# Kernel tuning notes

Hardware: AMD Instinct MI355X
Metric: run time of the kernel (lower is better)

The kernel has to match this reference:

```python
import jax, jax.numpy as jnp
import numpy as np

EPS_BN = 1e-5
EPS_NORM = 1e-12
TOP_K = 512


def _conv(x, w):
    # NCHW conv, stride 1, SAME padding (ultralytics Conv autopad)
    return jax.lax.conv_general_dilated(x, w, (1, 1), 'SAME',
                                        dimension_numbers=('NCHW', 'OIHW', 'NCHW'))


def _bn(x, g, b, m, v):
    # inference-mode BatchNorm2d
    inv = jax.lax.rsqrt(v + EPS_BN)
    return (x - m[None, :, None, None]) * (g * inv)[None, :, None, None] + b[None, :, None, None]


def _descriptor(feat, p):
    (w_dr, g_dr, b_dr, m_dr, v_dr,
     w_d1, g_d1, b_d1, m_d1, v_d1,
     g_e, b_e, m_e, v_e,
     w_d2, g_d2, b_d2, m_d2, v_d2) = p
    # dim_reduce: Conv(channel, channel//2, 1) = conv+BN+SiLU
    x = jax.nn.silu(_bn(_conv(feat, w_dr), g_dr, b_dr, m_dr, v_dr))
    # descriptor: Conv(c/2, c/2, 3) + BN + ReLU + Conv(c/2, c/4, 1)
    x = jax.nn.silu(_bn(_conv(x, w_d1), g_d1, b_d1, m_d1, v_d1))
    x = jax.nn.relu(_bn(x, g_e, b_e, m_e, v_e))
    x = jax.nn.silu(_bn(_conv(x, w_d2), g_d2, b_d2, m_d2, v_d2))
    return x


def _keypoints(desc):
    b, c, h, w = desc.shape
    resp = jnp.sqrt(jnp.sum(desc * desc, axis=1)).reshape(b, h * w)  # L2 norm over channels
    _, idx = jax.lax.top_k(resp, TOP_K)                              # [b, K]
    y = (idx // w).astype(desc.dtype) / (h - 1) * 2 - 1
    x = (idx % w).astype(desc.dtype) / (w - 1) * 2 - 1
    return jnp.stack([x, y], axis=-1), idx                           # [b,K,2], [b,K]


def _forward(rgb_feat, ir_feat, params):
    rgb_desc = _descriptor(rgb_feat, params)
    ir_desc = _descriptor(ir_feat, params)

    kp1, idx1 = _keypoints(rgb_desc)
    kp2, idx2 = _keypoints(ir_desc)

    b, c, h, w = rgb_desc.shape
    hw = h * w
    d1 = rgb_desc.reshape(b, c, hw)
    d2 = ir_desc.reshape(b, c, hw)
    d1 = d1 / jnp.maximum(jnp.linalg.norm(d1, axis=1, keepdims=True), EPS_NORM)
    d2 = d2 / jnp.maximum(jnp.linalg.norm(d2, axis=1, keepdims=True), EPS_NORM)
    corr = jnp.einsum('bcn,bcm->bnm', d1, d2)     # [b, hw, hw]
    soft = jax.nn.softmax(corr, axis=-1)

    # scalar matching weight per keypoint pair (gather at keypoint locations)
    bidx = jnp.arange(b)[:, None]
    wts = soft[bidx, idx1, idx2]                  # [b, K]

    # vectorized DLT: A rows, two per point, weighted
    x1, y1 = kp1[..., 0], kp1[..., 1]
    x2, y2 = kp2[..., 0], kp2[..., 1]
    one = jnp.ones_like(x1)
    zer = jnp.zeros_like(x1)
    r1 = jnp.stack([x1, y1, one, zer, zer, zer, -x2 * x1, -x2 * y1, -x2], axis=-1)
    r2 = jnp.stack([zer, zer, zer, x1, y1, one, -y2 * x1, -y2 * y1, -y2], axis=-1)
    A = jnp.stack([r1, r2], axis=2) * wts[:, :, None, None]   # [b,K,2,9]
    A = A.reshape(b, 2 * TOP_K, 9)

    _, _, Vh = jnp.linalg.svd(A, full_matrices=False)          # Vh: [b,9,9]
    # torch.svd returns V; original takes V[-1] == last COLUMN of jax Vh
    H = Vh[:, :, -1].reshape(b, 3, 3)
    return H, rgb_desc, ir_desc


def setup_inputs() -> dict:
    key = jax.random.key(0)
    ks = jax.random.split(key, 8)
    B, C, Hh, Ww = 2, 256, 64, 64
    c2, c4 = C // 2, C // 4
    f32 = jnp.float32

    def bn_params(c):
        return (jnp.ones((c,), f32), jnp.zeros((c,), f32),
                jnp.zeros((c,), f32), jnp.ones((c,), f32))

    g_dr, b_dr, m_dr, v_dr = bn_params(c2)
    g_d1, b_d1, m_d1, v_d1 = bn_params(c2)
    g_e, b_e, m_e, v_e = bn_params(c2)
    g_d2, b_d2, m_d2, v_d2 = bn_params(c4)

    return {
        'rgb_feat': jax.random.normal(ks[0], (B, C, Hh, Ww), f32),
        'ir_feat': jax.random.normal(ks[1], (B, C, Hh, Ww), f32),
        'w_dr': jax.random.normal(ks[2], (c2, C, 1, 1), f32) * 0.05,
        'g_dr': g_dr, 'b_dr': b_dr, 'm_dr': m_dr, 'v_dr': v_dr,
        'w_d1': jax.random.normal(ks[3], (c2, c2, 3, 3), f32) * 0.05,
        'g_d1': g_d1, 'b_d1': b_d1, 'm_d1': m_d1, 'v_d1': v_d1,
        'g_e': g_e, 'b_e': b_e, 'm_e': m_e, 'v_e': v_e,
        'w_d2': jax.random.normal(ks[4], (c4, c2, 1, 1), f32) * 0.05,
        'g_d2': g_d2, 'b_d2': b_d2, 'm_d2': m_d2, 'v_d2': v_d2,
    }


def reference(rgb_feat, ir_feat,
              w_dr, g_dr, b_dr, m_dr, v_dr,
              w_d1, g_d1, b_d1, m_d1, v_d1,
              g_e, b_e, m_e, v_e,
              w_d2, g_d2, b_d2, m_d2, v_d2):
    params = (w_dr, g_dr, b_dr, m_dr, v_dr,
              w_d1, g_d1, b_d1, m_d1, v_d1,
              g_e, b_e, m_e, v_e,
              w_d2, g_d2, b_d2, m_d2, v_d2)
    return _forward(rgb_feat, ir_feat, params)
```

## Files before the change

kernel.cpp:

```cpp
#include <hip/hip_runtime.h>
#include <math.h>


#define HW4 4096
#define NIMG 4

#define OFF_X1   0L
#define OFF_X2   (OFF_X1 + 4L*128*4096)
#define OFF_RESP (OFF_X2 + 4L*128*4096)
#define OFF_INVN (OFF_RESP + 4L*4096)
#define OFF_TOPI (OFF_INVN + 4L*4096)
#define OFF_WTS  (OFF_TOPI + 4L*512)
#define OFF_A    (OFF_WTS + 2L*512)
#define OFF_QN   OFF_X1
#define OFF_PART (OFF_X1 + 65536L)

#define NSPLIT 16

__device__ __forceinline__ float silu_f(float y) { return y / (1.f + expf(-y)); }

__global__ __launch_bounds__(256) void fm_conv1(
    const float* __restrict__ rgb, const float* __restrict__ ir,
    const float* __restrict__ w, const float* __restrict__ g,
    const float* __restrict__ bb, const float* __restrict__ mm,
    const float* __restrict__ vv, float* __restrict__ x1) {
  __shared__ float wl[256*8];
  int bid = blockIdx.x;
  int pblk = bid & 3, ocg = (bid >> 2) & 15, img = bid >> 6;
  int oc0 = ocg * 8;
  int tid = threadIdx.x;
  const float* src = (img < 2) ? (rgb + (long)img*256*HW4) : (ir + (long)(img-2)*256*HW4);
  for (int i = tid; i < 2048; i += 256) {
    int o = i & 7, ic = i >> 3;
    wl[i] = w[(oc0 + o)*256 + ic];
  }
  __syncthreads();
  int p0 = pblk*1024 + tid*4;
  float acc[8][4];
  #pragma unroll
  for (int o = 0; o < 8; ++o)
    #pragma unroll
    for (int j = 0; j < 4; ++j) acc[o][j] = 0.f;
  #pragma unroll 4
  for (int ic = 0; ic < 256; ++ic) {
    float4 v = *(const float4*)(src + (long)ic*HW4 + p0);
    float4 wa = *(const float4*)&wl[ic*8];
    float4 wb = *(const float4*)&wl[ic*8 + 4];
    acc[0][0] = fmaf(wa.x, v.x, acc[0][0]); acc[0][1] = fmaf(wa.x, v.y, acc[0][1]);
    acc[0][2] = fmaf(wa.x, v.z, acc[0][2]); acc[0][3] = fmaf(wa.x, v.w, acc[0][3]);
    acc[1][0] = fmaf(wa.y, v.x, acc[1][0]); acc[1][1] = fmaf(wa.y, v.y, acc[1][1]);
    acc[1][2] = fmaf(wa.y, v.z, acc[1][2]); acc[1][3] = fmaf(wa.y, v.w, acc[1][3]);
    acc[2][0] = fmaf(wa.z, v.x, acc[2][0]); acc[2][1] = fmaf(wa.z, v.y, acc[2][1]);
    acc[2][2] = fmaf(wa.z, v.z, acc[2][2]); acc[2][3] = fmaf(wa.z, v.w, acc[2][3]);
    acc[3][0] = fmaf(wa.w, v.x, acc[3][0]); acc[3][1] = fmaf(wa.w, v.y, acc[3][1]);
    acc[3][2] = fmaf(wa.w, v.z, acc[3][2]); acc[3][3] = fmaf(wa.w, v.w, acc[3][3]);
    acc[4][0] = fmaf(wb.x, v.x, acc[4][0]); acc[4][1] = fmaf(wb.x, v.y, acc[4][1]);
    acc[4][2] = fmaf(wb.x, v.z, acc[4][2]); acc[4][3] = fmaf(wb.x, v.w, acc[4][3]);
    acc[5][0] = fmaf(wb.y, v.x, acc[5][0]); acc[5][1] = fmaf(wb.y, v.y, acc[5][1]);
    acc[5][2] = fmaf(wb.y, v.z, acc[5][2]); acc[5][3] = fmaf(wb.y, v.w, acc[5][3]);
    acc[6][0] = fmaf(wb.z, v.x, acc[6][0]); acc[6][1] = fmaf(wb.z, v.y, acc[6][1]);
    acc[6][2] = fmaf(wb.z, v.z, acc[6][2]); acc[6][3] = fmaf(wb.z, v.w, acc[6][3]);
    acc[7][0] = fmaf(wb.w, v.x, acc[7][0]); acc[7][1] = fmaf(wb.w, v.y, acc[7][1]);
    acc[7][2] = fmaf(wb.w, v.z, acc[7][2]); acc[7][3] = fmaf(wb.w, v.w, acc[7][3]);
  }
  #pragma unroll
  for (int o = 0; o < 8; ++o) {
    int oc = oc0 + o;
    float inv = 1.f / sqrtf(vv[oc] + 1e-5f);
    float sc = g[oc]*inv;
    float4 r;
    r.x = silu_f((acc[o][0] - mm[oc])*sc + bb[oc]);
    r.y = silu_f((acc[o][1] - mm[oc])*sc + bb[oc]);
    r.z = silu_f((acc[o][2] - mm[oc])*sc + bb[oc]);
    r.w = silu_f((acc[o][3] - mm[oc])*sc + bb[oc]);
    *(float4*)(x1 + ((long)img*128 + oc)*HW4 + p0) = r;
  }
}

#define C3_TW 72
#define C3_TR 18
__global__ __launch_bounds__(256) void fm_conv3(
    const float* __restrict__ x1, const float* __restrict__ w,
    const float* __restrict__ g1, const float* __restrict__ b1,
    const float* __restrict__ m1, const float* __restrict__ v1,
    const float* __restrict__ ge, const float* __restrict__ be,
    const float* __restrict__ me, const float* __restrict__ ve,
    float* __restrict__ x2) {
  __shared__ float t[2][4][C3_TR*C3_TW];
  __shared__ float wl[2][4][9][8];
  int bid = blockIdx.x;
  int rt = bid & 3, ocg = (bid >> 2) & 15, img = bid >> 6;
  int oc0 = ocg * 8;
  int y0 = rt * 16;
  int tid = threadIdx.x;
  int ly = tid >> 4;
  int lx = tid & 15;
  int x0 = lx * 4;
  const float* xim = x1 + (long)img*128*HW4;

  for (int i = tid; i < 1152; i += 256) {
    int buf = i / 576, rem = i - buf*576;
    int q = rem / 144, rem2 = rem - q*144;
    int rr = rem2 >> 3, e = rem2 & 7;
    t[buf][q][rr*C3_TW + ((e < 4) ? e : 64 + e)] = 0.f;
  }

  int lofs4[5];
  int goff4[5];
  #pragma unroll
  for (int t5 = 0; t5 < 5; ++t5) {
    int i = tid + 256*t5;
    if (i < 1152) {
      int q = i / 288, rem = i - q*288;
      int r = rem >> 4, s4 = rem & 15;
      int gy = y0 + r - 1;
      lofs4[t5] = q*324 + r*18 + 1 + s4;
      goff4[t5] = (gy >= 0 && gy < 64) ? (q*1024 + gy*16 + s4) : -1;
    } else { lofs4[t5] = -1; goff4[t5] = -1; }
  }
  int wg0 = -1, wl0 = 0, wg1 = -1, wl1 = 0;
  {
    int i = tid;
    if (i < 288) {
      int o = i & 7, k = (i >> 3) % 9, q = i / 72;
      wg0 = ((oc0 + o)*128 + q)*9 + k;
      wl0 = (q*9 + k)*8 + o;
    }
    i = tid + 256;
    if (i < 288) {
      int o = i & 7, k = (i >> 3) % 9, q = i / 72;
      wg1 = ((oc0 + o)*128 + q)*9 + k;
      wl1 = (q*9 + k)*8 + o;
    }
  }

  float4 sreg[5];
  float wreg0 = 0.f, wreg1 = 0.f;

  #define C3_LOAD(IC0) do {                                              \
    const float4* f4b = (const float4*)xim + (long)(IC0)*1024;           \
    _Pragma("unroll")                                                    \
    for (int t5 = 0; t5 < 5; ++t5)                                       \
      sreg[t5] = (goff4[t5] >= 0) ? f4b[goff4[t5]]                       \
                                  : make_float4(0.f, 0.f, 0.f, 0.f);     \
    if (wg0 >= 0) wreg0 = w[(long)(IC0)*9 + wg0];                        \
    if (wg1 >= 0) wreg1 = w[(long)(IC0)*9 + wg1];                        \
  } while (0)

  #define C3_WRITE(BUF) do {                                             \
    float4* tb4 = (float4*)&t[BUF][0][0];                                \
    _Pragma("unroll")                                                    \
    for (int t5 = 0; t5 < 5; ++t5)                                       \
      if (lofs4[t5] >= 0) tb4[lofs4[t5]] = sreg[t5];                     \
    if (wg0 >= 0) (&wl[BUF][0][0][0])[wl0] = wreg0;                      \
    if (wg1 >= 0) (&wl[BUF][0][0][0])[wl1] = wreg1;                      \
  } while (0)

  float acc[8][4];
  #pragma unroll
  for (int o = 0; o < 8; ++o)
    #pragma unroll
    for (int j = 0; j < 4; ++j) acc[o][j] = 0.f;

  C3_LOAD(0);
  C3_WRITE(0);
  __syncthreads();
  int pb = 0;
  for (int ic0 = 0; ic0 < 128; ic0 += 4) {
    if (ic0 + 4 < 128) C3_LOAD(ic0 + 4);
    #pragma unroll
    for (int q = 0; q < 4; ++q) {
      const float* tq = &t[pb][q][0];
      float n0[3], n5v[3];
      float4 a1[3];
      #pragma unroll
      for (int dy = 0; dy < 3; ++dy) {
        int base = (ly + dy)*C3_TW + x0;
        a1[dy] = *(const float4*)(tq + base + 4);
        n0[dy]  = tq[base + 3];
        n5v[dy] = tq[base + 8];
      }
      #pragma unroll
      for (int k = 0; k < 9; ++k) {
        const int dy = k / 3, dx = k % 3;
        float4 wA = *(const float4*)&wl[pb][q][k][0];
        float4 wB = *(const float4*)&wl[pb][q][k][4];
        #pragma unroll
        for (int j = 0; j < 4; ++j) {
          const int c = dx + j;
          float nv = (c == 0) ? n0[dy] :
                     (c == 1) ? a1[dy].x :
                     (c == 2) ? a1[dy].y :
                     (c == 3) ? a1[dy].z :
                     (c == 4) ? a1[dy].w : n5v[dy];
          acc[0][j] = fmaf(wA.x, nv, acc[0][j]);
          acc[1][j] = fmaf(wA.y, nv, acc[1][j]);
          acc[2][j] = fmaf(wA.z, nv, acc[2][j]);
          acc[3][j] = fmaf(wA.w, nv, acc[3][j]);
          acc[4][j] = fmaf(wB.x, nv, acc[4][j]);
          acc[5][j] = fmaf(wB.y, nv, acc[5][j]);
          acc[6][j] = fmaf(wB.z, nv, acc[6][j]);
          acc[7][j] = fmaf(wB.w, nv, acc[7][j]);
        }
      }
    }
    if (ic0 + 4 < 128) C3_WRITE(pb ^ 1);
    __syncthreads();
    pb ^= 1;
  }
  int prow = (y0 + ly)*64 + x0;
  #pragma unroll
  for (int o = 0; o < 8; ++o) {
    int oc = oc0 + o;
    float inv1 = 1.f / sqrtf(v1[oc] + 1e-5f);
    float s1 = g1[oc]*inv1;
    float inve = 1.f / sqrtf(ve[oc] + 1e-5f);
    float s2 = ge[oc]*inve;
    float4 r;
    float y;
    y = silu_f((acc[o][0] - m1[oc])*s1 + b1[oc]); r.x = fmaxf((y - me[oc])*s2 + be[oc], 0.f);
    y = silu_f((acc[o][1] - m1[oc])*s1 + b1[oc]); r.y = fmaxf((y - me[oc])*s2 + be[oc], 0.f);
    y = silu_f((acc[o][2] - m1[oc])*s1 + b1[oc]); r.z = fmaxf((y - me[oc])*s2 + be[oc], 0.f);
    y = silu_f((acc[o][3] - m1[oc])*s1 + b1[oc]); r.w = fmaxf((y - me[oc])*s2 + be[oc], 0.f);
    *(float4*)(x2 + ((long)img*128 + oc)*HW4 + prow) = r;
  }
}

__global__ __launch_bounds__(256) void fm_conv2(
    const float* __restrict__ x2, const float* __restrict__ w,
    const float* __restrict__ g, const float* __restrict__ bb,
    const float* __restrict__ mm, const float* __restrict__ vv,
    float* __restrict__ out) {
  __shared__ float wl[128*4];
  int bid = blockIdx.x;
  int pblk = bid & 3, ocg = (bid >> 2) & 15, img = bid >> 6;
  int oc0 = ocg * 4;
  int tid = threadIdx.x;
  for (int i = tid; i < 512; i += 256) {
    int o = i & 3, ic = i >> 2;
    wl[i] = w[(oc0 + o)*128 + ic];
  }
  __syncthreads();
  int p0 = pblk*1024 + tid*4;
  const float* src = x2 + (long)img*128*HW4;
  float acc[4][4];
  #pragma unroll
  for (int o = 0; o < 4; ++o)
    #pragma unroll
    for (int j = 0; j < 4; ++j) acc[o][j] = 0.f;
  #pragma unroll 4
  for (int ic = 0; ic < 128; ++ic) {
    float4 v = *(const float4*)(src + (long)ic*HW4 + p0);
    float4 wa = *(const float4*)&wl[ic*4];
    acc[0][0] = fmaf(wa.x, v.x, acc[0][0]); acc[0][1] = fmaf(wa.x, v.y, acc[0][1]);
    acc[0][2] = fmaf(wa.x, v.z, acc[0][2]); acc[0][3] = fmaf(wa.x, v.w, acc[0][3]);
    acc[1][0] = fmaf(wa.y, v.x, acc[1][0]); acc[1][1] = fmaf(wa.y, v.y, acc[1][1]);
    acc[1][2] = fmaf(wa.y, v.z, acc[1][2]); acc[1][3] = fmaf(wa.y, v.w, acc[1][3]);
    acc[2][0] = fmaf(wa.z, v.x, acc[2][0]); acc[2][1] = fmaf(wa.z, v.y, acc[2][1]);
    acc[2][2] = fmaf(wa.z, v.z, acc[2][2]); acc[2][3] = fmaf(wa.z, v.w, acc[2][3]);
    acc[3][0] = fmaf(wa.w, v.x, acc[3][0]); acc[3][1] = fmaf(wa.w, v.y, acc[3][1]);
    acc[3][2] = fmaf(wa.w, v.z, acc[3][2]); acc[3][3] = fmaf(wa.w, v.w, acc[3][3]);
  }
  #pragma unroll
  for (int o = 0; o < 4; ++o) {
    int oc = oc0 + o;
    float inv = 1.f / sqrtf(vv[oc] + 1e-5f);
    float sc = g[oc]*inv;
    float* dst = out + 18 + (long)img*262144 + (long)oc*HW4 + p0;
    #pragma unroll
    for (int j = 0; j < 4; ++j)
      dst[j] = silu_f((acc[o][j] - mm[oc])*sc + bb[oc]);
  }
}

__global__ __launch_bounds__(256) void fm_resp(
    const float* __restrict__ out, float* __restrict__ resp, float* __restrict__ invn) {
  int t = blockIdx.x*256 + threadIdx.x;
  if (t >= NIMG*HW4) return;
  int img = t >> 12, p = t & 4095;
  const float* d = out + 18 + (long)img*262144;
  float s = 0.f;
  #pragma unroll
  for (int c = 0; c < 64; ++c) { float x = d[c*HW4 + p]; s = fmaf(x, x, s); }
  float r = sqrtf(s);
  resp[t] = r;
  invn[t] = 1.f / fmaxf(r, 1e-12f);
}

__global__ __launch_bounds__(1024) void fm_sort(
    const float* __restrict__ resp, int* __restrict__ topidx) {
  __shared__ unsigned long long keys[4096];
  int img = blockIdx.x, tid = threadIdx.x;
  const float* r = resp + (long)img*HW4;
  for (int i = tid; i < 4096; i += 1024) {
    unsigned int vb = __float_as_uint(r[i]);
    keys[i] = ((unsigned long long)vb << 32) | (unsigned int)(4095 - i);
  }
  __syncthreads();
  for (int k = 2; k <= 4096; k <<= 1) {
    for (int j = k >> 1; j > 0; j >>= 1) {
      for (int t = tid; t < 2048; t += 1024) {
        int i = 2*t - (t & (j - 1));
        int ixj = i ^ j;
        bool up = ((i & k) == 0);
        unsigned long long a = keys[i], b = keys[ixj];
        if ((a < b) == up) { keys[i] = b; keys[ixj] = a; }
      }
      __syncthreads();
    }
  }
  if (tid < 512) topidx[img*512 + tid] = 4095 - (int)(keys[tid] & 0xFFFFFFFFull);
}

__global__ __launch_bounds__(256) void fm_qgather(
    const float* __restrict__ out, const float* __restrict__ invn,
    const int* __restrict__ topidx, float* __restrict__ qn) {
  int tid = threadIdx.x;
  int kp = blockIdx.x*4 + (tid >> 6);
  int c = tid & 63;
  int b = kp >> 9, k = kp & 511;
  int row = topidx[b*512 + k];
  const float* d1 = out + 18 + (long)b*262144;
  qn[(long)kp*64 + c] = d1[c*HW4 + row] * invn[(long)b*HW4 + row];
}

__global__ __launch_bounds__(256) void fm_corr(
    const float* __restrict__ out, const float* __restrict__ invn,
    const float* __restrict__ qn, float* __restrict__ part) {
  __shared__ float Qs[32*64];
  __shared__ float Ds[64*128];
  int tid = threadIdx.x;
  int tx = tid & 31, ty = tid >> 5;
  int jsplit = blockIdx.x;
  int kg = blockIdx.y;
  int b = blockIdx.z;
  int k0 = kg*32;
  const float* d2 = out + 18 + (long)(2 + b)*262144;
  const float* in2 = invn + (long)(2 + b)*HW4;
  {
    const float4* src = (const float4*)(qn + ((long)b*512 + k0)*64);
    float4* dst = (float4*)Qs;
    dst[tid] = src[tid];
    dst[tid + 256] = src[tid + 256];
  }
  float m[4], s[4];
  #pragma unroll
  for (int r = 0; r < 4; ++r) { m[r] = -INFINITY; s[r] = 0.f; }
  #pragma unroll
  for (int tile = 0; tile < 2; ++tile) {
    int j0 = jsplit*256 + tile*128;
    __syncthreads();
    {
      float4* dst = (float4*)Ds;
      #pragma unroll
      for (int t = 0; t < 8; ++t) {
        int i = tid + 256*t;
        int c = i >> 5, col4 = i & 31;
        dst[i] = *(const float4*)(d2 + (long)c*HW4 + j0 + col4*4);
      }
    }
    __syncthreads();
    float acc[4][4];
    #pragma unroll
    for (int r = 0; r < 4; ++r)
      #pragma unroll
      for (int cc = 0; cc < 4; ++cc) acc[r][cc] = 0.f;
    const float4* Ds4 = (const float4*)Ds;
    #pragma unroll 4
    for (int c = 0; c < 64; ++c) {
      float4 dv = Ds4[c*32 + tx];
      #pragma unroll
      for (int r = 0; r < 4; ++r) {
        float qv = Qs[(ty*4 + r)*64 + c];
        acc[r][0] = fmaf(qv, dv.x, acc[r][0]);
        acc[r][1] = fmaf(qv, dv.y, acc[r][1]);
        acc[r][2] = fmaf(qv, dv.z, acc[r][2]);
        acc[r][3] = fmaf(qv, dv.w, acc[r][3]);
      }
    }
    float i0 = in2[j0 + tx*4 + 0];
    float i1 = in2[j0 + tx*4 + 1];
    float i2 = in2[j0 + tx*4 + 2];
    float i3 = in2[j0 + tx*4 + 3];
    #pragma unroll
    for (int r = 0; r < 4; ++r) {
      float v0 = acc[r][0]*i0, v1 = acc[r][1]*i1, v2 = acc[r][2]*i2, v3 = acc[r][3]*i3;
      float vm = fmaxf(fmaxf(v0, v1), fmaxf(v2, v3));
      float nm = fmaxf(m[r], vm);
      s[r] = s[r]*expf(m[r] - nm) + expf(v0 - nm) + expf(v1 - nm) + expf(v2 - nm) + expf(v3 - nm);
      m[r] = nm;
    }
  }
  #pragma unroll
  for (int off = 1; off < 32; off <<= 1) {
    #pragma unroll
    for (int r = 0; r < 4; ++r) {
      float om = __shfl_xor(m[r], off);
      float os = __shfl_xor(s[r], off);
      float nm = fmaxf(m[r], om);
      s[r] = s[r]*expf(m[r] - nm) + os*expf(om - nm);
      m[r] = nm;
    }
  }
  if (tx == 0) {
    #pragma unroll
    for (int r = 0; r < 4; ++r) {
      long idx = (((long)b*512 + k0 + ty*4 + r)*NSPLIT + jsplit)*2;
      part[idx] = m[r];
      part[idx + 1] = s[r];
    }
  }
}

__global__ __launch_bounds__(256) void fm_comb(
    const float* __restrict__ out, const float* __restrict__ invn,
    const int* __restrict__ topidx, const float* __restrict__ qn,
    const float* __restrict__ part, float* __restrict__ wts) {
  int tid = threadIdx.x;
  int kp = blockIdx.x*4 + (tid >> 6);
  int lane = tid & 63;
  int b = kp >> 9, k = kp & 511;
  int col = topidx[(2 + b)*512 + k];
  const float* d2 = out + 18 + (long)(2 + b)*262144;
  float dot = qn[(long)kp*64 + lane] * d2[lane*HW4 + col];
  #pragma unroll
  for (int off = 1; off < 64; off <<= 1) dot += __shfl_xor(dot, off);
  if (lane == 0) {
    const float* pp = part + (long)kp*NSPLIT*2;
    float M = -INFINITY;
    #pragma unroll
    for (int i = 0; i < NSPLIT; ++i) M = fmaxf(M, pp[2*i]);
    float S = 0.f;
    #pragma unroll
    for (int i = 0; i < NSPLIT; ++i) S += pp[2*i + 1]*expf(pp[2*i] - M);
    float v = dot * invn[(long)(2 + b)*HW4 + col];
    wts[b*512 + k] = expf(v - M)/S;
  }
}

__global__ __launch_bounds__(256) void fm_build(
    const int* __restrict__ topidx, const float* __restrict__ wts,
    float* __restrict__ A) {
  int t = blockIdx.x*256 + threadIdx.x;
  if (t >= 1024) return;
  int b = t >> 9, k = t & 511;
  int i1 = topidx[b*512 + k], i2 = topidx[(2 + b)*512 + k];
  float w = wts[b*512 + k];
  float x1 = (float)(i1 & 63) / 63.f * 2.f - 1.f;
  float y1 = (float)(i1 >> 6) / 63.f * 2.f - 1.f;
  float x2 = (float)(i2 & 63) / 63.f * 2.f - 1.f;
  float y2 = (float)(i2 >> 6) / 63.f * 2.f - 1.f;
  float* r = A + ((long)b*1024 + 2*k)*9;
  r[0] = x1*w;  r[1] = y1*w;  r[2] = w;
  r[3] = 0.f;   r[4] = 0.f;   r[5] = 0.f;
  r[6] = (-x2*x1)*w; r[7] = (-x2*y1)*w; r[8] = (-x2)*w;
  r[9]  = 0.f;  r[10] = 0.f;  r[11] = 0.f;
  r[12] = x1*w; r[13] = y1*w; r[14] = w;
  r[15] = (-y2*x1)*w; r[16] = (-y2*y1)*w; r[17] = (-y2)*w;
}

__device__ __forceinline__ void lap_slartg(float f, float g, float* cs, float* sn, float* r) {
  if (g == 0.f) { *cs = 1.f; *sn = 0.f; *r = f; }
  else if (f == 0.f) { *cs = 0.f; *sn = copysignf(1.f, g); *r = fabsf(g); }
  else {
    float d = sqrtf(f*f + g*g);
    *cs = fabsf(f) / d;
    *r = copysignf(d, f);
    *sn = g / (*r);
  }
}

__device__ __forceinline__ void lap_slas2(float f, float g, float h, float* ssmin, float* ssmax) {
  float fa = fabsf(f), ga = fabsf(g), ha = fabsf(h);
  float fhmn = fminf(fa, ha), fhmx = fmaxf(fa, ha);
  if (fhmn == 0.f) {
    *ssmin = 0.f;
    if (fhmx == 0.f) *ssmax = ga;
    else {
      float mx = fmaxf(fhmx, ga), mn = fminf(fhmx, ga);
      float q = mn / mx;
      *ssmax = mx * sqrtf(1.f + q*q);
    }
  } else {
    if (ga < fhmx) {
      float as_ = 1.f + fhmn/fhmx;
      float at_ = (fhmx - fhmn)/fhmx;
      float au = ga/fhmx; au = au*au;
      float c = 2.f / (sqrtf(as_*as_ + au) + sqrtf(at_*at_ + au));
      *ssmin = fhmn*c;
      *ssmax = fhmx/c;
    } else {
      float au = fhmx/ga;
      if (au == 0.f) { *ssmin = (fhmn*fhmx)/ga; *ssmax = ga; }
      else {
        float as_ = 1.f + fhmn/fhmx;
        float at_ = (fhmx - fhmn)/fhmx;
        float t1 = as_*au, t2 = at_*au;
        float c = 1.f / (sqrtf(1.f + t1*t1) + sqrtf(1.f + t2*t2));
        float smn = (fhmn*c)*au;
        *ssmin = smn + smn;
        *ssmax = ga/(c + c);
      }
    }
  }
}

__device__ __forceinline__ void lap_slasv2(float f, float g, float h, float* ssmin, float* ssmax,
                           float* snr, float* csr, float* snl, float* csl) {
  const float epsv = 5.9604645e-08f;
  float ft = f, fa = fabsf(f), ht = h, ha = fabsf(h);
  int pmax = 1;
  bool swap_ = (ha > fa);
  if (swap_) { pmax = 3; float tmp = ft; ft = ht; ht = tmp; tmp = fa; fa = ha; ha = tmp; }
  float gt = g, ga = fabsf(gt);
  float clt = 0.f, crt = 0.f, slt = 0.f, srt = 0.f;
  if (ga == 0.f) { *ssmin = ha; *ssmax = fa; clt = 1.f; crt = 1.f; slt = 0.f; srt = 0.f; }
  else {
    bool gasmal = true;
    if (ga > fa) {
      pmax = 2;
      if ((fa/ga) < epsv) {
        gasmal = false;
        *ssmax = ga;
        if (ha > 1.f) *ssmin = fa/(ga/ha); else *ssmin = (fa/ga)*ha;
        clt = 1.f; slt = ht/gt; srt = 1.f; crt = ft/gt;
      }
    }
    if (gasmal) {
      float d = fa - ha, l;
      if (d == fa) l = 1.f; else l = d/fa;
      float m_ = gt/ft;
      float t = 2.f - l;
      float mm2 = m_*m_, tt = t*t;
      float s = sqrtf(tt + mm2);
      float r_ = (l == 0.f) ? fabsf(m_) : sqrtf(l*l + mm2);
      float a = 0.5f*(s + r_);
      *ssmin = ha/a;
      *ssmax = fa*a;
      if (mm2 == 0.f) {
        if (l == 0.f) t = copysignf(2.f, ft)*copysignf(1.f, gt);
        else t = gt/copysignf(d, ft) + m_/t;
      } else {
        t = (m_/(s + t) + m_/(r_ + l))*(1.f + a);
      }
      float l2 = sqrtf(t*t + 4.f);
      crt = 2.f/l2;
      srt = t/l2;
      clt = (crt + srt*m_)/a;
      slt = (ht/ft)*srt/a;
    }
  }
  if (swap_) { *csl = srt; *snl = crt; *csr = slt; *snr = clt; }
  else { *csl = clt; *snl = slt; *csr = crt; *snr = srt; }
  float tsign = 1.f;
  if (pmax == 1) tsign = copysignf(1.f, *csr)*copysignf(1.f, *csl)*copysignf(1.f, f);
  if (pmax == 2) tsign = copysignf(1.f, *snr)*copysignf(1.f, *csl)*copysignf(1.f, g);
  if (pmax == 3) tsign = copysignf(1.f, *snr)*copysignf(1.f, *snl)*copysignf(1.f, h);
  *ssmax = copysignf(*ssmax, tsign);
  *ssmin = copysignf(*ssmin, tsign*copysignf(1.f, f)*copysignf(1.f, h));
}

__device__ __forceinline__ float get9(const float (&a)[9], int idx) {
  float v = a[0];
#pragma unroll
  for (int i = 1; i < 9; ++i) if (idx == i) v = a[i];
  return v;
}
__device__ __forceinline__ void set9(float (&a)[9], int idx, float val) {
#pragma unroll
  for (int i = 0; i < 9; ++i) if (idx == i) a[i] = val;
}

__device__ __forceinline__ void bdsqr9_reg(float (&dd)[9], float (&ee)[9], float (&vt)[9]) {
  const float eps_ = 5.9604645e-08f;
  const float unfl_ = 1.17549435e-38f;
  const float tol_ = 10.f*eps_;
  float sminoa = fabsf(dd[0]);
  if (sminoa != 0.f) {
    float mu = sminoa;
    bool z = false;
#pragma unroll
    for (int i = 1; i < 9; ++i) {
      if (!z) {
        mu = fabsf(dd[i])*(mu/(mu + fabsf(ee[i-1])));
        sminoa = fminf(sminoa, mu);
        if (sminoa == 0.f) z = true;
      }
    }
  }
  sminoa = sminoa / 3.f;
  float thresh = fmaxf(tol_*sminoa, 486.f*unfl_);
  int m = 9, iter = 0, oldll = -1, oldm = -1, idir = 0;
  float sminl = 0.f;
  int guard = 0;
  while (guard++ < 2000) {
    if (m <= 1) break;
    if (iter > 486) break;
    float smax = fabsf(get9(dd, m-1));
    int ll = 0; bool split = false;
#pragma unroll
    for (int l2 = 8; l2 >= 1; --l2) {
      if (l2 <= m - 1 && !split) {
        float abss = fabsf(dd[l2-1]);
        float abse = fabsf(ee[l2-1]);
        if (abse <= thresh) { ll = l2; split = true; }
        else smax = fmaxf(smax, fmaxf(abss, abse));
      }
    }
    if (split) {
      set9(ee, ll-1, 0.f);
      if (ll == m - 1) { m = m - 1; continue; }
    } else ll = 0;
    ll = ll + 1;
    if (ll == m - 1) {
      float d1 = get9(dd, m-2), e1 = get9(ee, m-2), d2v = get9(dd, m-1);
      float sigmn, sigmx, sinr, cosr, sinl_, cosl_;
      lap_slasv2(d1, e1, d2v, &sigmn, &sigmx, &sinr, &cosr, &sinl_, &cosl_);
      set9(dd, m-2, sigmx); set9(ee, m-2, 0.f); set9(dd, m-1, sigmn);
      float xt = get9(vt, m-2), yt = get9(vt, m-1);
      set9(vt, m-2, cosr*xt + sinr*yt);
      set9(vt, m-1, cosr*yt - sinr*xt);
      m -= 2; continue;
    }
    if (ll > oldm || m < oldll)
      idir = (fabsf(get9(dd, ll-1)) >= fabsf(get9(dd, m-1))) ? 1 : 2;
    bool conv = false;
    if (idir == 1) {
      if (fabsf(get9(ee, m-2)) <= tol_*fabsf(get9(dd, m-1))) { set9(ee, m-2, 0.f); continue; }
      float mu = fabsf(get9(dd, ll-1));
      sminl = mu;
#pragma unroll
      for (int lll = 1; lll <= 8; ++lll) {
        if (lll >= ll && lll <= m - 1 && !conv) {
          if (fabsf(ee[lll-1]) <= tol_*mu) { ee[lll-1] = 0.f; conv = true; }
          else {
            mu = fabsf(dd[lll])*(mu/(mu + fabsf(ee[lll-1])));
            sminl = fminf(sminl, mu);
          }
        }
      }
    } else {
      if (fabsf(get9(ee, ll-1)) <= tol_*fabsf(get9(dd, ll-1))) { set9(ee, ll-1, 0.f); continue; }
      float mu = fabsf(get9(dd, m-1));
      sminl = mu;
#pragma unroll
      for (int lll = 8; lll >= 1; --lll) {
        if (lll <= m - 1 && lll >= ll && !conv) {
          if (fabsf(ee[lll-1]) <= tol_*mu) { ee[lll-1] = 0.f; conv = true; }
          else {
            mu = fabsf(dd[lll-1])*(mu/(mu + fabsf(ee[lll-1])));
            sminl = fminf(sminl, mu);
          }
        }
      }
    }
    if (conv) continue;
    oldll = ll; oldm = m;
    float shift = 0.f, rdum;
    if (!(9.f*tol_*(sminl/smax) <= fmaxf(eps_, 0.01f*tol_))) {
      float sll;
      if (idir == 1) { sll = fabsf(get9(dd, ll-1)); lap_slas2(get9(dd, m-2), get9(ee, m-2), get9(dd, m-1), &shift, &rdum); }
      else           { sll = fabsf(get9(dd, m-1));  lap_slas2(get9(dd, ll-1), get9(ee, ll-1), get9(dd, ll), &shift, &rdum); }
      if (sll > 0.f) { float q = shift/sll; if (q*q < eps_) shift = 0.f; }
    }
    iter += m - ll;
    if (shift == 0.f) {
      if (idir == 1) {
        float cs = 1.f, oldcs = 1.f, sn = 0.f, oldsn = 0.f, r;
#pragma unroll
        for (int i = 1; i <= 8; ++i) {
          if (i >= ll && i <= m - 1) {
            lap_slartg(dd[i-1]*cs, ee[i-1], &cs, &sn, &r);
            if (i >= 2 && i > ll) ee[i-2] = oldsn*r;
            float dn;
            lap_slartg(oldcs*r, dd[i]*sn, &oldcs, &oldsn, &dn);
            dd[i-1] = dn;
            float t = vt[i]; vt[i] = cs*t - sn*vt[i-1]; vt[i-1] = sn*t + cs*vt[i-1];
          }
        }
        float h2 = get9(dd, m-1)*cs;
        set9(dd, m-1, h2*oldcs);
        set9(ee, m-2, h2*oldsn);
        if (fabsf(get9(ee, m-2)) <= thresh) set9(ee, m-2, 0.f);
      } else {
        float cs = 1.f, oldcs = 1.f, sn = 0.f, oldsn = 0.f, r;
#pragma unroll
        for (int i = 9; i >= 2; --i) {
          if (i <= m && i >= ll + 1) {
            lap_slartg(dd[i-1]*cs, ee[i-2], &cs, &sn, &r);
            if (i < m) ee[i-1] = oldsn*r;
            float dn;
            lap_slartg(oldcs*r, dd[i-2]*sn, &oldcs, &oldsn, &dn);
            dd[i-1] = dn;
            float c2 = oldcs, s2 = -oldsn;
            float t = vt[i-1]; vt[i-1] = c2*t - s2*vt[i-2]; vt[i-2] = s2*t + c2*vt[i-2];
          }
        }
        float h2 = get9(dd, ll-1)*cs;
        set9(dd, ll-1, h2*oldcs);
        set9(ee, ll-1, h2*oldsn);
        if (fabsf(get9(ee, ll-1)) <= thresh) set9(ee, ll-1, 0.f);
      }
    } else {
      if (idir == 1) {
        float d0 = get9(dd, ll-1);
        float f2 = (fabsf(d0) - shift)*(copysignf(1.f, d0) + shift/d0);
        float g2 = get9(ee, ll-1);
#pragma unroll
        for (int i = 1; i <= 8; ++i) {
          if (i >= ll && i <= m - 1) {
            float cr, sr, cl, sl, r;
            lap_slartg(f2, g2, &cr, &sr, &r);
            if (i >= 2 && i > ll) ee[i-2] = r;
            f2 = cr*dd[i-1] + sr*ee[i-1];
            ee[i-1] = cr*ee[i-1] - sr*dd[i-1];
            g2 = sr*dd[i];
            dd[i] = cr*dd[i];
            lap_slartg(f2, g2, &cl, &sl, &r);
            dd[i-1] = r;
            f2 = cl*ee[i-1] + sl*dd[i];
            dd[i] = cl*dd[i] - sl*ee[i-1];
            if (i < m - 1) { g2 = sl*ee[i]; ee[i] = cl*ee[i]; }
            float t = vt[i]; vt[i] = cr*t - sr*vt[i-1]; vt[i-1] = sr*t + cr*vt[i-1];
          }
        }
        set9(ee, m-2, f2);
        if (fabsf(get9(ee, m-2)) <= thresh) set9(ee, m-2, 0.f);
      } else {
        float dm = get9(dd, m-1);
        float f2 = (fabsf(dm) - shift)*(copysignf(1.f, dm) + shift/dm);
        float g2 = get9(ee, m-2);
#pragma unroll
        for (int i = 9; i >= 2; --i) {
          if (i <= m && i >= ll + 1) {
            float cr, sr, cl, sl, r;
            lap_slartg(f2, g2, &cr, &sr, &r);
            if (i < m) ee[i-1] = r;
            f2 = cr*dd[i-1] + sr*ee[i-2];
            ee[i-2] = cr*ee[i-2] - sr*dd[i-1];
            g2 = sr*dd[i-2];
            dd[i-2] = cr*dd[i-2];
            lap_slartg(f2, g2, &cl, &sl, &r);
            dd[i-1] = r;
            f2 = cl*ee[i-2] + sl*dd[i-2];
            dd[i-2] = cl*dd[i-2] - sl*ee[i-2];
            if (i >= 3 && i > ll + 1) { g2 = sl*ee[i-3]; ee[i-3] = cl*ee[i-3]; }
            float c2 = cl, s2 = -sl;
            float t = vt[i-1]; vt[i-1] = c2*t - s2*vt[i-2]; vt[i-2] = s2*t + c2*vt[i-2];
          }
        }
        set9(ee, ll-1, f2);
        if (fabsf(get9(ee, ll-1)) <= thresh) set9(ee, ll-1, 0.f);
      }
    }
  }
#pragma unroll
  for (int i = 0; i < 9; ++i) {
    if (dd[i] < 0.f) { dd[i] = -dd[i]; vt[i] = -vt[i]; }
  }
#pragma unroll
  for (int i = 1; i <= 8; ++i) {
    int isub = 1; float smin2 = dd[0];
#pragma unroll
    for (int j = 2; j <= 9; ++j) {
      if (j <= 10 - i) {
        if (dd[j-1] <= smin2) { isub = j; smin2 = dd[j-1]; }
      }
    }
    const int tgt = 10 - i;
    if (isub != tgt) {
      set9(dd, isub-1, dd[tgt-1]);
      dd[tgt-1] = smin2;
      float tv = get9(vt, isub-1);
      set9(vt, isub-1, vt[tgt-1]);
      vt[tgt-1] = tv;
    }
  }
}

__global__ __launch_bounds__(256) void fm_svd(
    const float* __restrict__ Aglob, float* __restrict__ outH) {
  __shared__ float As[1024*9];
  __shared__ float wred[4][12];
  __shared__ float bc[4];
  int b = blockIdx.x, tid = threadIdx.x;
  int wv = tid >> 6, ln = tid & 63;
  const float* Ab = Aglob + (long)b*9216;
  {
    const float4* s4 = (const float4*)Ab;
    float4* d4 = (float4*)As;
#pragma unroll
    for (int t = 0; t < 9; ++t) d4[tid + 256*t] = s4[tid + 256*t];
  }
  __syncthreads();
  for (int k = 0; k < 9; ++k) {
    float ps = 0.f;
    for (int r = k + 1 + tid; r < 1024; r += 256) {
      float x = As[r*9 + k]; ps = fmaf(x, x, ps);
    }
#pragma unroll
    for (int off = 1; off < 64; off <<= 1) ps += __shfl_xor(ps, off);
    if (ln == 0) wred[wv][8] = ps;
    __syncthreads();
    if (tid == 0) {
      float ssq = wred[0][8] + wred[1][8] + wred[2][8] + wred[3][8];
      float alpha = As[k*9 + k];
      float tau = 0.f, sc = 0.f, beta = alpha;
      if (ssq != 0.f) {
        beta = -copysignf(sqrtf(alpha*alpha + ssq), alpha);
        tau = (beta - alpha)/beta;
        sc = 1.f/(alpha - beta);
      }
      bc[0] = tau; bc[1] = sc; bc[2] = beta;
    }
    __syncthreads();
    float tau = bc[0], sc = bc[1];
    if (tau != 0.f) {
      for (int r = k + 1 + tid; r < 1024; r += 256) As[r*9 + k] *= sc;
    }
    __syncthreads();
    if (tau != 0.f) {
      float pd[8];
#pragma unroll
      for (int jj = 0; jj < 8; ++jj) pd[jj] = 0.f;
      for (int r = k + 1 + tid; r < 1024; r += 256) {
        float vk = As[r*9 + k];
#pragma unroll
        for (int jj = 0; jj < 8; ++jj) {
          int j = k + 1 + jj;
          if (j < 9) pd[jj] = fmaf(vk, As[r*9 + j], pd[jj]);
        }
      }
#pragma unroll
      for (int off = 1; off < 64; off <<= 1) {
#pragma unroll
        for (int jj = 0; jj < 8; ++jj) pd[jj] += __shfl_xor(pd[jj], off);
      }
      if (ln == 0) {
#pragma unroll
        for (int jj = 0; jj < 8; ++jj) wred[wv][jj] = pd[jj];
      }
      __syncthreads();
      float sj[8];
#pragma unroll
      for (int jj = 0; jj < 8; ++jj) {
        int j = k + 1 + jj;
        float v = 0.f;
        if (j < 9)
          v = (wred[0][jj] + wred[1][jj] + wred[2][jj] + wred[3][jj] + As[k*9 + j]) * tau;
        sj[jj] = v;
      }
      for (int r = k + 1 + tid; r < 1024; r += 256) {
        float vk = As[r*9 + k];
#pragma unroll
        for (int jj = 0; jj < 8; ++jj) {
          int j = k + 1 + jj;
          if (j < 9) As[r*9 + j] -= sj[jj]*vk;
        }
      }
      __syncthreads();
      if (tid == 0) {
#pragma unroll
        for (int jj = 0; jj < 8; ++jj) {
          int j = k + 1 + jj;
          if (j < 9) As[k*9 + j] -= sj[jj];
        }
      }
    }
    if (tid == 0) As[k*9 + k] = bc[2];
    __syncthreads();
  }
  if (tid < 64) {
    float R[9][9];
#pragma unroll
    for (int i = 0; i < 9; ++i)
#pragma unroll
      for (int j = 0; j < 9; ++j)
        R[i][j] = (j >= i) ? As[i*9 + j] : 0.f;
    float dd[9], ee[9], taupv[8], pt8[9];
    ee[8] = 0.f;
#pragma unroll
    for (int i = 0; i < 9; ++i) {
      float alpha = R[i][i];
      float ssq = 0.f;
#pragma unroll
      for (int r2 = i + 1; r2 < 9; ++r2) ssq += R[r2][i]*R[r2][i];
      float tauq = 0.f, beta = alpha;
      if (ssq != 0.f) {
        beta = -copysignf(sqrtf(alpha*alpha + ssq), alpha);
        tauq = (beta - alpha)/beta;
        float scq = 1.f/(alpha - beta);
#pragma unroll
        for (int r2 = i + 1; r2 < 9; ++r2) R[r2][i] *= scq;
      }
      dd[i] = beta;
      if (tauq != 0.f) {
#pragma unroll
        for (int j = i + 1; j < 9; ++j) {
          float s = R[i][j];
#pragma unroll
          for (int r2 = i + 1; r2 < 9; ++r2) s += R[r2][i]*R[r2][j];
          s *= tauq;
          R[i][j] -= s;
#pragma unroll
          for (int r2 = i + 1; r2 < 9; ++r2) R[r2][j] -= s*R[r2][i];
        }
      }
      if (i < 8) {
        float alpha2 = R[i][i+1];
        float ssq2 = 0.f;
#pragma unroll
        for (int c = i + 2; c < 9; ++c) ssq2 += R[i][c]*R[i][c];
        float tp = 0.f, beta2 = alpha2;
        if (ssq2 != 0.f) {
          beta2 = -copysignf(sqrtf(alpha2*alpha2 + ssq2), alpha2);
          tp = (beta2 - alpha2)/beta2;
          float scp = 1.f/(alpha2 - beta2);
#pragma unroll
          for (int c = i + 2; c < 9; ++c) R[i][c] *= scp;
        }
        ee[i] = beta2;
        taupv[i] = tp;
        if (tp != 0.f) {
#pragma unroll
          for (int r2 = i + 1; r2 < 9; ++r2) {
            float s = R[r2][i+1];
#pragma unroll
            for (int c = i + 2; c < 9; ++c) s += R[i][c]*R[r2][c];
            s *= tp;
            R[r2][i+1] -= s;
#pragma unroll
            for (int c = i + 2; c < 9; ++c) R[r2][c] -= s*R[i][c];
          }
        }
      }
    }
#pragma unroll
    for (int i = 0; i < 9; ++i) pt8[i] = (i == 8) ? 1.f : 0.f;
#pragma unroll
    for (int i = 0; i < 8; ++i) {
      float tp = taupv[i];
      if (tp != 0.f) {
        float s = pt8[i+1];
#pragma unroll
        for (int r2 = i + 2; r2 < 9; ++r2) s += R[i][r2]*pt8[r2];
        s *= tp;
        pt8[i+1] -= s;
#pragma unroll
        for (int r2 = i + 2; r2 < 9; ++r2) pt8[r2] -= s*R[i][r2];
      }
    }
    float vt[9];
#pragma unroll
    for (int i = 0; i < 9; ++i) vt[i] = (i == tid) ? 1.f : 0.f;
    bdsqr9_reg(dd, ee, vt);
    float p8 = (tid < 9) ? get9(pt8, tid) : 0.f;
    float h[9];
#pragma unroll
    for (int i = 0; i < 9; ++i) h[i] = vt[i]*p8;
#pragma unroll
    for (int off = 1; off < 16; off <<= 1) {
#pragma unroll
      for (int i = 0; i < 9; ++i) h[i] += __shfl_xor(h[i], off);
    }
    if (tid == 0) {
#pragma unroll
      for (int i = 0; i < 9; ++i) outH[b*9 + i] = h[i];
    }
  }
}

extern "C" void kernel_launch(void* const* d_in, const int* in_sizes, int n_in,
                              void* d_out, int out_size, void* d_ws, size_t ws_size,
                              hipStream_t stream) {
  const float* rgb  = (const float*)d_in[0];
  const float* ir   = (const float*)d_in[1];
  const float* w_dr = (const float*)d_in[2];
  const float* g_dr = (const float*)d_in[3];
  const float* b_dr = (const float*)d_in[4];
  const float* m_dr = (const float*)d_in[5];
  const float* v_dr = (const float*)d_in[6];
  const float* w_d1 = (const float*)d_in[7];
  const float* g_d1 = (const float*)d_in[8];
  const float* b_d1 = (const float*)d_in[9];
  const float* m_d1 = (const float*)d_in[10];
  const float* v_d1 = (const float*)d_in[11];
  const float* g_e  = (const float*)d_in[12];
  const float* b_e  = (const float*)d_in[13];
  const float* m_e  = (const float*)d_in[14];
  const float* v_e  = (const float*)d_in[15];
  const float* w_d2 = (const float*)d_in[16];
  const float* g_d2 = (const float*)d_in[17];
  const float* b_d2 = (const float*)d_in[18];
  const float* m_d2 = (const float*)d_in[19];
  const float* v_d2 = (const float*)d_in[20];

  float* out = (float*)d_out;
  float* ws  = (float*)d_ws;
  float* x1   = ws + OFF_X1;
  float* x2   = ws + OFF_X2;
  float* resp = ws + OFF_RESP;
  float* invn = ws + OFF_INVN;
  int*   topi = (int*)(ws + OFF_TOPI);
  float* wts  = ws + OFF_WTS;
  float* Amat = ws + OFF_A;
  float* qn   = ws + OFF_QN;
  float* part = ws + OFF_PART;

  fm_conv1<<<256, 256, 0, stream>>>(rgb, ir, w_dr, g_dr, b_dr, m_dr, v_dr, x1);
  fm_conv3<<<256, 256, 0, stream>>>(x1, w_d1, g_d1, b_d1, m_d1, v_d1,
                                    g_e, b_e, m_e, v_e, x2);
  fm_conv2<<<256, 256, 0, stream>>>(x2, w_d2, g_d2, b_d2, m_d2, v_d2, out);
  fm_resp<<<(NIMG*HW4 + 255)/256, 256, 0, stream>>>(out, resp, invn);
  fm_sort<<<NIMG, 1024, 0, stream>>>(resp, topi);
  fm_qgather<<<256, 256, 0, stream>>>(out, invn, topi, qn);
  fm_corr<<<dim3(NSPLIT, 16, 2), 256, 0, stream>>>(out, invn, qn, part);
  fm_comb<<<256, 256, 0, stream>>>(out, invn, topi, qn, part, wts);
  fm_build<<<4, 256, 0, stream>>>(topi, wts, Amat);
  fm_svd<<<2, 256, 0, stream>>>(Amat, out);
}
```

Baseline: 394.4 us.

## Halve per-thread pixel tiles in conv kernels and use shuffles for 3x3 halo

The three convolution kernels now give each thread two pixels instead of four, which doubles the grid to 512 blocks so more of the GPU's compute units are busy. The 3x3 conv drops the padded shared-memory halo columns and the zero-fill pass, and gets left and right neighbours through wavefront shuffles with zero at the row edges. This lowers register pressure and shared-memory footprint. In exchange, each weight load from shared memory now feeds fewer FMAs, and the narrower float2 global accesses may lower memory efficiency.

Result: slower. 413.6 us (+4.9%).

```diff
diff --git a/kernel.cpp b/kernel.cpp
--- a/kernel.cpp
+++ b/kernel.cpp
@@ -26,7 +26,7 @@
     const float* __restrict__ vv, float* __restrict__ x1) {
   __shared__ float wl[256*8];
   int bid = blockIdx.x;
-  int pblk = bid & 3, ocg = (bid >> 2) & 15, img = bid >> 6;
+  int pblk = bid & 7, ocg = (bid >> 3) & 15, img = bid >> 7;
   int oc0 = ocg * 8;
   int tid = threadIdx.x;
   const float* src = (img < 2) ? (rgb + (long)img*256*HW4) : (ir + (long)(img-2)*256*HW4);
@@ -35,50 +35,37 @@
     wl[i] = w[(oc0 + o)*256 + ic];
   }
   __syncthreads();
-  int p0 = pblk*1024 + tid*4;
-  float acc[8][4];
-  #pragma unroll
-  for (int o = 0; o < 8; ++o)
-    #pragma unroll
-    for (int j = 0; j < 4; ++j) acc[o][j] = 0.f;
+  int p0 = pblk*512 + tid*2;
+  float acc[8][2];
+  #pragma unroll
+  for (int o = 0; o < 8; ++o) { acc[o][0] = 0.f; acc[o][1] = 0.f; }
   #pragma unroll 4
   for (int ic = 0; ic < 256; ++ic) {
-    float4 v = *(const float4*)(src + (long)ic*HW4 + p0);
+    float2 v = *(const float2*)(src + (long)ic*HW4 + p0);
     float4 wa = *(const float4*)&wl[ic*8];
     float4 wb = *(const float4*)&wl[ic*8 + 4];
     acc[0][0] = fmaf(wa.x, v.x, acc[0][0]); acc[0][1] = fmaf(wa.x, v.y, acc[0][1]);
-    acc[0][2] = fmaf(wa.x, v.z, acc[0][2]); acc[0][3] = fmaf(wa.x, v.w, acc[0][3]);
     acc[1][0] = fmaf(wa.y, v.x, acc[1][0]); acc[1][1] = fmaf(wa.y, v.y, acc[1][1]);
-    acc[1][2] = fmaf(wa.y, v.z, acc[1][2]); acc[1][3] = fmaf(wa.y, v.w, acc[1][3]);
     acc[2][0] = fmaf(wa.z, v.x, acc[2][0]); acc[2][1] = fmaf(wa.z, v.y, acc[2][1]);
-    acc[2][2] = fmaf(wa.z, v.z, acc[2][2]); acc[2][3] = fmaf(wa.z, v.w, acc[2][3]);
     acc[3][0] = fmaf(wa.w, v.x, acc[3][0]); acc[3][1] = fmaf(wa.w, v.y, acc[3][1]);
-    acc[3][2] = fmaf(wa.w, v.z, acc[3][2]); acc[3][3] = fmaf(wa.w, v.w, acc[3][3]);
     acc[4][0] = fmaf(wb.x, v.x, acc[4][0]); acc[4][1] = fmaf(wb.x, v.y, acc[4][1]);
-    acc[4][2] = fmaf(wb.x, v.z, acc[4][2]); acc[4][3] = fmaf(wb.x, v.w, acc[4][3]);
     acc[5][0] = fmaf(wb.y, v.x, acc[5][0]); acc[5][1] = fmaf(wb.y, v.y, acc[5][1]);
-    acc[5][2] = fmaf(wb.y, v.z, acc[5][2]); acc[5][3] = fmaf(wb.y, v.w, acc[5][3]);
     acc[6][0] = fmaf(wb.z, v.x, acc[6][0]); acc[6][1] = fmaf(wb.z, v.y, acc[6][1]);
-    acc[6][2] = fmaf(wb.z, v.z, acc[6][2]); acc[6][3] = fmaf(wb.z, v.w, acc[6][3]);
     acc[7][0] = fmaf(wb.w, v.x, acc[7][0]); acc[7][1] = fmaf(wb.w, v.y, acc[7][1]);
-    acc[7][2] = fmaf(wb.w, v.z, acc[7][2]); acc[7][3] = fmaf(wb.w, v.w, acc[7][3]);
   }
   #pragma unroll
   for (int o = 0; o < 8; ++o) {
     int oc = oc0 + o;
     float inv = 1.f / sqrtf(vv[oc] + 1e-5f);
     float sc = g[oc]*inv;
-    float4 r;
+    float2 r;
     r.x = silu_f((acc[o][0] - mm[oc])*sc + bb[oc]);
     r.y = silu_f((acc[o][1] - mm[oc])*sc + bb[oc]);
-    r.z = silu_f((acc[o][2] - mm[oc])*sc + bb[oc]);
-    r.w = silu_f((acc[o][3] - mm[oc])*sc + bb[oc]);
-    *(float4*)(x1 + ((long)img*128 + oc)*HW4 + p0) = r;
-  }
-}
-
-#define C3_TW 72
-#define C3_TR 18
+    *(float2*)(x1 + ((long)img*128 + oc)*HW4 + p0) = r;
+  }
+}
+
+#define C3_ROWS 10
 __global__ __launch_bounds__(256) void fm_conv3(
     const float* __restrict__ x1, const float* __restrict__ w,
     const float* __restrict__ g1, const float* __restrict__ b1,
@@ -86,37 +73,28 @@
     const float* __restrict__ ge, const float* __restrict__ be,
     const float* __restrict__ me, const float* __restrict__ ve,
     float* __restrict__ x2) {
-  __shared__ float t[2][4][C3_TR*C3_TW];
+  __shared__ float t[2][4][C3_ROWS*64];
   __shared__ float wl[2][4][9][8];
   int bid = blockIdx.x;
-  int rt = bid & 3, ocg = (bid >> 2) & 15, img = bid >> 6;
+  int rt = bid & 7, ocg = (bid >> 3) & 15, img = bid >> 7;
   int oc0 = ocg * 8;
-  int y0 = rt * 16;
+  int y0 = rt * 8;
   int tid = threadIdx.x;
-  int ly = tid >> 4;
-  int lx = tid & 15;
-  int x0 = lx * 4;
+  int ly = tid >> 5;
+  int lx = tid & 31;
+  int x0 = lx * 2;
   const float* xim = x1 + (long)img*128*HW4;
 
-  for (int i = tid; i < 1152; i += 256) {
-    int buf = i / 576, rem = i - buf*576;
-    int q = rem / 144, rem2 = rem - q*144;
-    int rr = rem2 >> 3, e = rem2 & 7;
-    t[buf][q][rr*C3_TW + ((e < 4) ? e : 64 + e)] = 0.f;
-  }
-
-  int lofs4[5];
-  int goff4[5];
-  #pragma unroll
-  for (int t5 = 0; t5 < 5; ++t5) {
+  int goff4[3];
+  #pragma unroll
+  for (int t5 = 0; t5 < 3; ++t5) {
     int i = tid + 256*t5;
-    if (i < 1152) {
-      int q = i / 288, rem = i - q*288;
+    if (i < 640) {
+      int q = i / 160, rem = i - q*160;
       int r = rem >> 4, s4 = rem & 15;
       int gy = y0 + r - 1;
-      lofs4[t5] = q*324 + r*18 + 1 + s4;
       goff4[t5] = (gy >= 0 && gy < 64) ? (q*1024 + gy*16 + s4) : -1;
-    } else { lofs4[t5] = -1; goff4[t5] = -1; }
+    } else goff4[t5] = -2;
   }
   int wg0 = -1, wl0 = 0, wg1 = -1, wl1 = 0;
   {
@@ -134,13 +112,13 @@
     }
   }
 
-  float4 sreg[5];
+  float4 sreg[3];
   float wreg0 = 0.f, wreg1 = 0.f;
 
   #define C3_LOAD(IC0) do {                                              \
     const float4* f4b = (const float4*)xim + (long)(IC0)*1024;           \
     _Pragma("unroll")                                                    \
-    for (int t5 = 0; t5 < 5; ++t5)                                       \
+    for (int t5 = 0; t5 < 3; ++t5)                                       \
       sreg[t5] = (goff4[t5] >= 0) ? f4b[goff4[t5]]                       \
                                   : make_float4(0.f, 0.f, 0.f, 0.f);     \
     if (wg0 >= 0) wreg0 = w[(long)(IC0)*9 + wg0];                        \
@@ -150,17 +128,17 @@
   #define C3_WRITE(BUF) do {                                             \
     float4* tb4 = (float4*)&t[BUF][0][0];                                \
     _Pragma("unroll")                                                    \
-    for (int t5 = 0; t5 < 5; ++t5)                                       \
-      if (lofs4[t5] >= 0) tb4[lofs4[t5]] = sreg[t5];                     \
+    for (int t5 = 0; t5 < 3; ++t5) {                                     \
+      int i = tid + 256*t5;                                              \
+      if (goff4[t5] != -2) tb4[i] = sreg[t5];                            \
+    }                                                                    \
     if (wg0 >= 0) (&wl[BUF][0][0][0])[wl0] = wreg0;                      \
     if (wg1 >= 0) (&wl[BUF][0][0][0])[wl1] = wreg1;                      \
   } while (0)
 
-  float acc[8][4];
-  #pragma unroll
-  for (int o = 0; o < 8; ++o)
-    #pragma unroll
-    for (int j = 0; j < 4; ++j) acc[o][j] = 0.f;
+  float acc[8][2];
+  #pragma unroll
+  for (int o = 0; o < 8; ++o) { acc[o][0] = 0.f; acc[o][1] = 0.f; }
 
   C3_LOAD(0);
   C3_WRITE(0);
@@ -171,14 +149,14 @@
     #pragma unroll
     for (int q = 0; q < 4; ++q) {
       const float* tq = &t[pb][q][0];
-      float n0[3], n5v[3];
-      float4 a1[3];
+      float2 a1[3]; float n0[3], n5[3];
       #pragma unroll
       for (int dy = 0; dy < 3; ++dy) {
-        int base = (ly + dy)*C3_TW + x0;
-        a1[dy] = *(const float4*)(tq + base + 4);
-        n0[dy]  = tq[base + 3];
-        n5v[dy] = tq[base + 8];
+        a1[dy] = *(const float2*)(tq + (ly + dy)*64 + x0);
+        float up = __shfl_up(a1[dy].y, 1, 32);
+        float dn = __shfl_down(a1[dy].x, 1, 32);
+        n0[dy] = (lx == 0)  ? 0.f : up;
+        n5[dy] = (lx == 31) ? 0.f : dn;
       }
       #pragma unroll
       for (int k = 0; k < 9; ++k) {
@@ -186,13 +164,11 @@
         float4 wA = *(const float4*)&wl[pb][q][k][0];
         float4 wB = *(const float4*)&wl[pb][q][k][4];
         #pragma unroll
-        for (int j = 0; j < 4; ++j) {
+        for (int j = 0; j < 2; ++j) {
           const int c = dx + j;
           float nv = (c == 0) ? n0[dy] :
                      (c == 1) ? a1[dy].x :
-                     (c == 2) ? a1[dy].y :
-                     (c == 3) ? a1[dy].z :
-                     (c == 4) ? a1[dy].w : n5v[dy];
+                     (c == 2) ? a1[dy].y : n5[dy];
           acc[0][j] = fmaf(wA.x, nv, acc[0][j]);
           acc[1][j] = fmaf(wA.y, nv, acc[1][j]);
           acc[2][j] = fmaf(wA.z, nv, acc[2][j]);
@@ -216,13 +192,11 @@
     float s1 = g1[oc]*inv1;
     float inve = 1.f / sqrtf(ve[oc] + 1e-5f);
     float s2 = ge[oc]*inve;
-    float4 r;
+    float2 r;
     float y;
     y = silu_f((acc[o][0] - m1[oc])*s1 + b1[oc]); r.x = fmaxf((y - me[oc])*s2 + be[oc], 0.f);
     y = silu_f((acc[o][1] - m1[oc])*s1 + b1[oc]); r.y = fmaxf((y - me[oc])*s2 + be[oc], 0.f);
-    y = silu_f((acc[o][2] - m1[oc])*s1 + b1[oc]); r.z = fmaxf((y - me[oc])*s2 + be[oc], 0.f);
-    y = silu_f((acc[o][3] - m1[oc])*s1 + b1[oc]); r.w = fmaxf((y - me[oc])*s2 + be[oc], 0.f);
-    *(float4*)(x2 + ((long)img*128 + oc)*HW4 + prow) = r;
+    *(float2*)(x2 + ((long)img*128 + oc)*HW4 + prow) = r;
   }
 }
 
@@ -233,7 +207,7 @@
     float* __restrict__ out) {
   __shared__ float wl[128*4];
   int bid = blockIdx.x;
-  int pblk = bid & 3, ocg = (bid >> 2) & 15, img = bid >> 6;
+  int pblk = bid & 7, ocg = (bid >> 3) & 15, img = bid >> 7;
   int oc0 = ocg * 4;
   int tid = threadIdx.x;
   for (int i = tid; i < 512; i += 256) {
@@ -241,25 +215,19 @@
     wl[i] = w[(oc0 + o)*128 + ic];
   }
   __syncthreads();
-  int p0 = pblk*1024 + tid*4;
+  int p0 = pblk*512 + tid*2;
   const float* src = x2 + (long)img*128*HW4;
-  float acc[4][4];
-  #pragma unroll
-  for (int o = 0; o < 4; ++o)
-    #pragma unroll
-    for (int j = 0; j < 4; ++j) acc[o][j] = 0.f;
+  float acc[4][2];
+  #pragma unroll
+  for (int o = 0; o < 4; ++o) { acc[o][0] = 0.f; acc[o][1] = 0.f; }
   #pragma unroll 4
   for (int ic = 0; ic < 128; ++ic) {
-    float4 v = *(const float4*)(src + (long)ic*HW4 + p0);
+    float2 v = *(const float2*)(src + (long)ic*HW4 + p0);
     float4 wa = *(const float4*)&wl[ic*4];
     acc[0][0] = fmaf(wa.x, v.x, acc[0][0]); acc[0][1] = fmaf(wa.x, v.y, acc[0][1]);
-    acc[0][2] = fmaf(wa.x, v.z, acc[0][2]); acc[0][3] = fmaf(wa.x, v.w, acc[0][3]);
     acc[1][0] = fmaf(wa.y, v.x, acc[1][0]); acc[1][1] = fmaf(wa.y, v.y, acc[1][1]);
-    acc[1][2] = fmaf(wa.y, v.z, acc[1][2]); acc[1][3] = fmaf(wa.y, v.w, acc[1][3]);
     acc[2][0] = fmaf(wa.z, v.x, acc[2][0]); acc[2][1] = fmaf(wa.z, v.y, acc[2][1]);
-    acc[2][2] = fmaf(wa.z, v.z, acc[2][2]); acc[2][3] = fmaf(wa.z, v.w, acc[2][3]);
     acc[3][0] = fmaf(wa.w, v.x, acc[3][0]); acc[3][1] = fmaf(wa.w, v.y, acc[3][1]);
-    acc[3][2] = fmaf(wa.w, v.z, acc[3][2]); acc[3][3] = fmaf(wa.w, v.w, acc[3][3]);
   }
   #pragma unroll
   for (int o = 0; o < 4; ++o) {
@@ -267,9 +235,8 @@
     float inv = 1.f / sqrtf(vv[oc] + 1e-5f);
     float sc = g[oc]*inv;
     float* dst = out + 18 + (long)img*262144 + (long)oc*HW4 + p0;
-    #pragma unroll
-    for (int j = 0; j < 4; ++j)
-      dst[j] = silu_f((acc[o][j] - mm[oc])*sc + bb[oc]);
+    dst[0] = silu_f((acc[o][0] - mm[oc])*sc + bb[oc]);
+    dst[1] = silu_f((acc[o][1] - mm[oc])*sc + bb[oc]);
   }
 }
 
@@ -1007,10 +974,10 @@
   float* qn   = ws + OFF_QN;
   float* part = ws + OFF_PART;
 
-  fm_conv1<<<256, 256, 0, stream>>>(rgb, ir, w_dr, g_dr, b_dr, m_dr, v_dr, x1);
-  fm_conv3<<<256, 256, 0, stream>>>(x1, w_d1, g_d1, b_d1, m_d1, v_d1,
+  fm_conv1<<<512, 256, 0, stream>>>(rgb, ir, w_dr, g_dr, b_dr, m_dr, v_dr, x1);
+  fm_conv3<<<512, 256, 0, stream>>>(x1, w_d1, g_d1, b_d1, m_d1, v_d1,
                                     g_e, b_e, m_e, v_e, x2);
-  fm_conv2<<<256, 256, 0, stream>>>(x2, w_d2, g_d2, b_d2, m_d2, v_d2, out);
+  fm_conv2<<<512, 256, 0, stream>>>(x2, w_d2, g_d2, b_d2, m_d2, v_d2, out);
   fm_resp<<<(NIMG*HW4 + 255)/256, 256, 0, stream>>>(out, resp, invn);
   fm_sort<<<NIMG, 1024, 0, stream>>>(resp, topi);
   fm_qgather<<<256, 256, 0, stream>>>(out, invn, topi, qn);
```
